# Optimization experiments

Measured on AMD Instinct MI355X. Metric: run time of the kernel, lower is better.

## Reference

```python
import jax, jax.numpy as jnp
import numpy as np

EPS = 1e-11


def setup_inputs() -> dict:
    key = jax.random.key(0)
    k1, k2, k3 = jax.random.split(key, 3)
    B, C, G, P = 32, 512, 16, 5
    z = jax.random.normal(k1, (B, C, G, G), dtype=jnp.float32)
    c = jax.random.normal(k2, (B, C, G, G), dtype=jnp.float32)
    # stacked 1x1 conv weights, one (C,C) matrix per prediction step
    W = jax.random.normal(k3, (P, C, C), dtype=jnp.float32) * 0.02
    return {"z": z, "c": c, "W": W, "neg_samples": 16, "skip_step": 1}


def reference(z, c, W, neg_samples, skip_step):
    B, C, G, _ = z.shape
    P = W.shape[0]
    total = jnp.float32(0.0)
    for k in range(1, P + 1):
        Gp = G - (k + skip_step)  # rows remaining after the k+skip offset
        # 1x1 conv == per-pixel matmul; permute(2,3,0,1) -> (Gp, G, B, C)
        ztwk = jnp.einsum('oc,bcij->ijbo', W[k - 1], z[:, :, k + skip_step:, :])
        N = Gp * G * B
        # random-index gather for negative sampling (fixed key per step)
        idx = jax.random.randint(jax.random.key(1000 + k), (N * neg_samples,), 0, N)
        ztwk_shuf = ztwk.reshape(N, C)[idx].reshape(Gp, G, B, neg_samples, C)
        # context c[:, :, :-(k+skip_step), :] permuted to (Gp, G, B, C)
        ctx = jnp.transpose(c[:, :, :Gp, :], (2, 3, 0, 1))
        # positive and negative dot products
        log_fk_main = jnp.einsum('ijbc,ijbc->ijb', ctx, ztwk)[..., None]  # (Gp,G,B,1)
        log_fk_shuf = jnp.einsum('ijbc,ijbnc->ijbn', ctx, ztwk_shuf)      # (Gp,G,B,neg)
        logits = jnp.concatenate([log_fk_main, log_fk_shuf], axis=3)
        probs = jax.nn.softmax(logits, axis=3)
        # ExpNLLLoss with target == 0 (the positive slot), mean reduction
        total = total - jnp.mean(jnp.log(probs[..., 0] + EPS))
    return total / P
```

## Files before the change

kernel.cpp:

```cpp
#include <hip/hip_runtime.h>
#include <stdint.h>


typedef __attribute__((ext_vector_type(4))) int i32x4;

using gld_gp = const __attribute__((address_space(1))) uint32_t*;
using gld_lp = __attribute__((address_space(3))) uint32_t*;

#if __has_builtin(__builtin_amdgcn_sdot4)
#define SDOT4(a, b, c) __builtin_amdgcn_sdot4((a), (b), (c), false)
#else
__device__ inline int sdot4_sw(int a, int b, int c) {
  c += (int)(signed char)(a) * (int)(signed char)(b);
  c += (int)(signed char)(a >> 8) * (int)(signed char)(b >> 8);
  c += (int)(signed char)(a >> 16) * (int)(signed char)(b >> 16);
  c += (int)(signed char)(a >> 24) * (int)(signed char)(b >> 24);
  return c;
}
#define SDOT4(a, b, c) sdot4_sw((a), (b), (c))
#endif

__host__ __device__ inline uint32_t rotl32(uint32_t x, int d) {
  return (x << d) | (x >> (32 - d));
}

__host__ __device__ inline void tf2x32(uint32_t k0, uint32_t k1,
                                       uint32_t x0, uint32_t x1,
                                       uint32_t& o0, uint32_t& o1) {
  uint32_t ks0 = k0, ks1 = k1, ks2 = 0x1BD11BDAu ^ k0 ^ k1;
  x0 += ks0; x1 += ks1;
#define TF_R(r) { x0 += x1; x1 = rotl32(x1, (r)); x1 ^= x0; }
  TF_R(13) TF_R(15) TF_R(26) TF_R(6)
  x0 += ks1; x1 += ks2 + 1u;
  TF_R(17) TF_R(29) TF_R(16) TF_R(24)
  x0 += ks2; x1 += ks0 + 2u;
  TF_R(13) TF_R(15) TF_R(26) TF_R(6)
  x0 += ks0; x1 += ks1 + 3u;
  TF_R(17) TF_R(29) TF_R(16) TF_R(24)
  x0 += ks1; x1 += ks2 + 4u;
  TF_R(13) TF_R(15) TF_R(26) TF_R(6)
  x0 += ks2; x1 += ks0 + 5u;
#undef TF_R
  o0 = x0; o1 = x1;
}

__device__ inline signed char f2i8(float f, float s) {
  int v = (int)rintf(f * s);
  v = v > 127 ? 127 : (v < -127 ? -127 : v);
  return (signed char)v;
}

struct KeyParams {
  uint32_t k1a[5], k1b[5], k2a[5], k2b[5], mult[5];
};

__global__ __launch_bounds__(256) void prep_kernel(const float* __restrict__ z,
                                                   const float* __restrict__ c,
                                                   const float* __restrict__ W,
                                                   signed char* __restrict__ zi8,
                                                   signed char* __restrict__ ci8,
                                                   signed char* __restrict__ Wti8,
                                                   int* __restrict__ idxb,
                                                   float* __restrict__ out,
                                                   KeyParams p) {
  int blk = blockIdx.x;
  int t = threadIdx.x;
  if (blk < 896) {
    bool isz = blk < 448;
    const float* src = isz ? z : c;
    signed char* dst = isz ? zi8 : ci8;
    int bb = isz ? blk : blk - 448;
    int g = isz ? 2 + (bb >> 5) : (bb >> 5);
    int b = bb & 31;
    __shared__ signed char tileB[512][17];
#pragma unroll 4
    for (int it = 0; it < 32; ++it) {
      int e = it * 256 + t;
      int cc = e >> 4, j = e & 15;
      tileB[cc][j] = f2i8(src[b * 131072 + cc * 256 + g * 16 + j], 32.f);
    }
    __syncthreads();
#pragma unroll 4
    for (int it = 0; it < 16; ++it) {
      int e = it * 256 + t;
      int jj = e >> 8, cc2 = (e & 255) * 2;
      char2 v = {tileB[cc2][jj], tileB[cc2 + 1][jj]};
      *reinterpret_cast<char2*>(
          &dst[(size_t)((g * 16 + jj) * 32 + b) * 512 + cc2]) = v;
    }
  } else if (blk < 1216) {
    int bb = blk - 896;
    int k = bb >> 6, rem = bb & 63;
    int ot = rem >> 3, it = rem & 7;
    const float* Wk = W + (size_t)k * 262144;
    signed char* Wo = Wti8 + (size_t)k * 262144;
    __shared__ signed char wt[64][68];
    int ii = t & 63, q0 = t >> 6;
#pragma unroll
    for (int q = 0; q < 16; ++q) {
      int oo = q0 + q * 4;
      wt[oo][ii] = f2i8(Wk[(size_t)(ot * 64 + oo) * 512 + it * 64 + ii], 1024.f);
    }
    __syncthreads();
    int oo2 = t & 63;
#pragma unroll
    for (int q = 0; q < 16; ++q) {
      int i2 = q0 + q * 4;
      Wo[(size_t)(it * 64 + i2) * 512 + ot * 64 + oo2] = wt[oo2][i2];
    }
  } else {
    int gid = (blk - 1216) * 256 + t;
    if (gid == 0) out[0] = 0.0f;
    int k; uint32_t span; int m;
    if (gid < 114688)      { k = 0; m = gid;          span = 7168; }
    else if (gid < 221184) { k = 1; m = gid - 114688; span = 6656; }
    else if (gid < 319488) { k = 2; m = gid - 221184; span = 6144; }
    else if (gid < 409600) { k = 3; m = gid - 319488; span = 5632; }
    else                   { k = 4; m = gid - 409600; span = 5120; }
    uint32_t h0, h1, l0, l1;
    tf2x32(p.k1a[k], p.k1b[k], 0u, (uint32_t)m, h0, h1);
    tf2x32(p.k2a[k], p.k2b[k], 0u, (uint32_t)m, l0, l1);
    uint32_t hi = h0 ^ h1, lo = l0 ^ l1;
    uint32_t off = ((hi % span) * p.mult[k] + (lo % span)) % span;
    idxb[gid] = (int)off;
  }
}

__global__ __launch_bounds__(256) void gemm_i8(const signed char* __restrict__ ci8,
                                               const signed char* __restrict__ Wti8,
                                               signed char* __restrict__ u) {
  int rt = blockIdx.x, ct = blockIdx.y;
  int kk, Tk;
  if (rt < 56)       { kk = 0; Tk = 0;   }
  else if (rt < 108) { kk = 1; Tk = 56;  }
  else if (rt < 156) { kk = 2; Tk = 108; }
  else if (rt < 200) { kk = 3; Tk = 156; }
  else               { kk = 4; Tk = 200; }
  const int preR[5] = {0, 7168, 13824, 19968, 25600};
  int r0 = (rt - Tk) * 128;
  const signed char* A  = ci8 + (size_t)r0 * 512;
  const signed char* Bw = Wti8 + (size_t)kk * 262144 + (size_t)ct * 128 * 512;
  signed char* Cb = u + ((size_t)preR[kk] + r0) * 512 + ct * 128;

  __shared__ __align__(1024) signed char As[8192];
  __shared__ __align__(1024) signed char Bs[8192];
  int tid = threadIdx.x;
  int wave = tid >> 6, lane = tid & 63;
  int wr = wave >> 1, wc = wave & 1;
  int lp = lane & 15, lg = lane >> 4;

  i32x4 acc[4][4];
#pragma unroll
  for (int m = 0; m < 4; ++m)
#pragma unroll
    for (int n = 0; n < 4; ++n) acc[m][n] = (i32x4){0, 0, 0, 0};

  int lrow = lane >> 2, lq = lane & 3;
  for (int c0 = 0; c0 < 512; c0 += 64) {
#pragma unroll
    for (int it = 0; it < 2; ++it) {
      int chunk = wave * 2 + it;
      int row = chunk * 16 + lrow;
      __builtin_amdgcn_global_load_lds(
          (gld_gp)(const void*)(A + (size_t)row * 512 + c0 + lq * 16),
          (gld_lp)(void*)(As + chunk * 1024 + lane * 16), 16, 0, 0);
      __builtin_amdgcn_global_load_lds(
          (gld_gp)(const void*)(Bw + (size_t)row * 512 + c0 + lq * 16),
          (gld_lp)(void*)(Bs + chunk * 1024 + lane * 16), 16, 0, 0);
    }
    __syncthreads();
    i32x4 af[4], bfr[4];
#pragma unroll
    for (int m = 0; m < 4; ++m)
      af[m] = *reinterpret_cast<const i32x4*>(&As[(wr * 64 + m * 16 + lp) * 64 + lg * 16]);
#pragma unroll
    for (int n = 0; n < 4; ++n)
      bfr[n] = *reinterpret_cast<const i32x4*>(&Bs[(wc * 64 + n * 16 + lp) * 64 + lg * 16]);
#pragma unroll
    for (int m = 0; m < 4; ++m)
#pragma unroll
      for (int n = 0; n < 4; ++n)
        acc[m][n] = __builtin_amdgcn_mfma_i32_16x16x64_i8(af[m], bfr[n], acc[m][n], 0, 0, 0);
    __syncthreads();
  }
#pragma unroll
  for (int m = 0; m < 4; ++m)
#pragma unroll
    for (int n = 0; n < 4; ++n)
#pragma unroll
      for (int j = 0; j < 4; ++j) {
        int row = wr * 64 + m * 16 + lg * 4 + j;
        int col = wc * 64 + n * 16 + lp;
        int q = (int)rintf((float)acc[m][n][j] * (1.f / 512.f));
        q = q > 127 ? 127 : (q < -127 ? -127 : q);
        Cb[(size_t)row * 512 + col] = (signed char)q;
      }
}

__device__ inline int dot16i8(uint4 u4, uint4 z4, int acc) {
  acc = SDOT4((int)u4.x, (int)z4.x, acc);
  acc = SDOT4((int)u4.y, (int)z4.y, acc);
  acc = SDOT4((int)u4.z, (int)z4.z, acc);
  acc = SDOT4((int)u4.w, (int)z4.w, acc);
  return acc;
}

__global__ __launch_bounds__(256) void loss_fused(const signed char* __restrict__ u,
                                                  const signed char* __restrict__ zi8,
                                                  const int* __restrict__ idxb,
                                                  float* __restrict__ out) {
  int tid = threadIdx.x;
  int wave = tid >> 6, lane = tid & 63;
  int g = lane >> 4, lp = lane & 15;
  int r = blockIdx.x * 16 + wave * 4 + g;

  int base, basez; float scale;
  if (r < 7168)       { base = 0;     basez = 1024; scale = 1.f / (7168.f * 5.f); }
  else if (r < 13824) { base = 7168;  basez = 1536; scale = 1.f / (6656.f * 5.f); }
  else if (r < 19968) { base = 13824; basez = 2048; scale = 1.f / (6144.f * 5.f); }
  else if (r < 25600) { base = 19968; basez = 2560; scale = 1.f / (5632.f * 5.f); }
  else                { base = 25600; basez = 3072; scale = 1.f / (5120.f * 5.f); }
  int rloc = r - base;

  uint4 uA, uB;
  {
    const uint4* u4 = reinterpret_cast<const uint4*>(&u[(size_t)r * 512 + lp * 32]);
    uA = u4[0]; uB = u4[1];
  }
  const int4* ip = reinterpret_cast<const int4*>(&idxb[(size_t)r * 16]);
  int4 i0 = ip[0], i1 = ip[1], i2 = ip[2], i3 = ip[3];
  int rn[16] = {i0.x, i0.y, i0.z, i0.w, i1.x, i1.y, i1.z, i1.w,
                i2.x, i2.y, i2.z, i2.w, i3.x, i3.y, i3.z, i3.w};

  int s[17];
  {
    const uint4* p0 = reinterpret_cast<const uint4*>(
        &zi8[(size_t)(basez + rloc) * 512 + lp * 32]);
    uint4 a = p0[0], b = p0[1];
    s[0] = dot16i8(uB, b, dot16i8(uA, a, 0));
  }
#pragma unroll
  for (int grp = 0; grp < 2; ++grp) {
    uint4 a0, b0, a1, b1, a2, b2, a3, b3, a4, b4, a5, b5, a6, b6, a7, b7;
#define LDROW(i, A, B)                                                        \
    {                                                                         \
      const uint4* p = reinterpret_cast<const uint4*>(                        \
          &zi8[(size_t)(basez + rn[grp * 8 + (i)]) * 512 + lp * 32]);         \
      A = p[0]; B = p[1];                                                     \
    }
    LDROW(0, a0, b0) LDROW(1, a1, b1) LDROW(2, a2, b2) LDROW(3, a3, b3)
    LDROW(4, a4, b4) LDROW(5, a5, b5) LDROW(6, a6, b6) LDROW(7, a7, b7)
#undef LDROW
    s[1 + grp * 8 + 0] = dot16i8(uB, b0, dot16i8(uA, a0, 0));
    s[1 + grp * 8 + 1] = dot16i8(uB, b1, dot16i8(uA, a1, 0));
    s[1 + grp * 8 + 2] = dot16i8(uB, b2, dot16i8(uA, a2, 0));
    s[1 + grp * 8 + 3] = dot16i8(uB, b3, dot16i8(uA, a3, 0));
    s[1 + grp * 8 + 4] = dot16i8(uB, b4, dot16i8(uA, a4, 0));
    s[1 + grp * 8 + 5] = dot16i8(uB, b5, dot16i8(uA, a5, 0));
    s[1 + grp * 8 + 6] = dot16i8(uB, b6, dot16i8(uA, a6, 0));
    s[1 + grp * 8 + 7] = dot16i8(uB, b7, dot16i8(uA, a7, 0));
  }
#pragma unroll
  for (int i = 0; i < 17; ++i) {
#pragma unroll
    for (int o = 8; o > 0; o >>= 1) s[i] += __shfl_xor(s[i], o, 64);
  }
  const float inv = 1.f / 2048.f;
  float sf[17];
#pragma unroll
  for (int i = 0; i < 17; ++i) sf[i] = (float)s[i] * inv;
  float mx = sf[0];
#pragma unroll
  for (int i = 1; i < 17; ++i) mx = fmaxf(mx, sf[i]);
  float se = 0.f;
#pragma unroll
  for (int i = 0; i < 17; ++i) se += __expf(sf[i] - mx);
  float p0 = __expf(sf[0] - mx) / se;
  float lsum = -logf(p0 + 1e-11f) * scale;

  __shared__ float red[16];
  if (lp == 0) red[wave * 4 + g] = lsum;
  __syncthreads();
  if (tid == 0) {
    float tsum = 0.f;
#pragma unroll
    for (int i = 0; i < 16; ++i) tsum += red[i];
    atomicAdd(out, tsum);
  }
}

extern "C" void kernel_launch(void* const* d_in, const int* in_sizes, int n_in,
                              void* d_out, int out_size, void* d_ws, size_t ws_size,
                              hipStream_t stream) {
  const float* z = (const float*)d_in[0];
  const float* c = (const float*)d_in[1];
  const float* W = (const float*)d_in[2];
  float* out = (float*)d_out;

  signed char* zi8  = (signed char*)d_ws;
  signed char* ci8  = zi8 + ((size_t)4 << 20);
  signed char* Wti8 = ci8 + ((size_t)4 << 20);
  signed char* u    = Wti8 + ((size_t)2 << 20);
  int* idxb = (int*)(u + (size_t)15728640);

  KeyParams p;
  for (int k = 1; k <= 5; ++k) {
    int Gp = 16 - (k + 1);
    uint32_t span = (uint32_t)(Gp * 512);
    p.mult[k - 1] = (uint32_t)((1ull << 32) % (uint64_t)span);
    uint32_t key0 = 0u, key1 = (uint32_t)(1000 + k);
    tf2x32(key0, key1, 0u, 0u, p.k1a[k - 1], p.k1b[k - 1]);
    tf2x32(key0, key1, 0u, 1u, p.k2a[k - 1], p.k2b[k - 1]);
  }

  prep_kernel<<<dim3(3136), dim3(256), 0, stream>>>(z, c, W, zi8, ci8, Wti8,
                                                    idxb, out, p);
  gemm_i8<<<dim3(240, 4), dim3(256), 0, stream>>>(ci8, Wti8, u);
  loss_fused<<<dim3(1920), dim3(256), 0, stream>>>(u, zi8, idxb, out);
}
```

Measured before the change: 136.2 us.

## Restructure z/c int8 transpose-quantize with packed 16-byte stores; add nontemporal hints

The prep stage now gives each block a 64-channel slice of one batch over all 256 pixels instead of one grid row across all channels. It packs four quantized channels per 32-bit word in shared memory and writes 16-byte vectors, skipping the rows the loss never reads. This gives coalesced float reads and wide stores and cuts the prep block count. Separately, the gemm output stores and the loss kernel's loads of u and the index buffer use nontemporal hints to reduce cache pollution, which could hurt if that data would otherwise hit in cache.

```diff
diff --git a/kernel.cpp b/kernel.cpp
--- a/kernel.cpp
+++ b/kernel.cpp
@@ -3,6 +3,7 @@
 
 
 typedef __attribute__((ext_vector_type(4))) int i32x4;
+typedef __attribute__((ext_vector_type(4))) unsigned int u32x4;
 
 using gld_gp = const __attribute__((address_space(1))) uint32_t*;
 using gld_lp = __attribute__((address_space(3))) uint32_t*;
@@ -65,31 +66,42 @@
                                                    KeyParams p) {
   int blk = blockIdx.x;
   int t = threadIdx.x;
-  if (blk < 896) {
-    bool isz = blk < 448;
-    const float* src = isz ? z : c;
+  if (blk < 512) {
+    bool isz = blk < 256;
+    int bb = isz ? blk : blk - 256;
+    int b = bb & 31;
+    int cc0 = (bb >> 5) * 64;
+    const float* src = (isz ? z : c) + (size_t)b * 131072 + (size_t)cc0 * 256;
     signed char* dst = isz ? zi8 : ci8;
-    int bb = isz ? blk : blk - 448;
-    int g = isz ? 2 + (bb >> 5) : (bb >> 5);
-    int b = bb & 31;
-    __shared__ signed char tileB[512][17];
-#pragma unroll 4
-    for (int it = 0; it < 32; ++it) {
-      int e = it * 256 + t;
-      int cc = e >> 4, j = e & 15;
-      tileB[cc][j] = f2i8(src[b * 131072 + cc * 256 + g * 16 + j], 32.f);
+    __shared__ uint32_t tileU[256 * 17];
+#pragma unroll
+    for (int w = 0; w < 16; ++w) {
+      uint32_t pk = 0;
+#pragma unroll
+      for (int e = 0; e < 4; ++e) {
+        float f = src[(size_t)(w * 4 + e) * 256 + t];
+        pk |= ((uint32_t)(uint8_t)f2i8(f, 32.f)) << (e * 8);
+      }
+      tileU[t * 17 + w] = pk;
     }
     __syncthreads();
-#pragma unroll 4
-    for (int it = 0; it < 16; ++it) {
-      int e = it * 256 + t;
-      int jj = e >> 8, cc2 = (e & 255) * 2;
-      char2 v = {tileB[cc2][jj], tileB[cc2 + 1][jj]};
-      *reinterpret_cast<char2*>(
-          &dst[(size_t)((g * 16 + jj) * 32 + b) * 512 + cc2]) = v;
-    }
-  } else if (blk < 1216) {
-    int bb = blk - 896;
+#pragma unroll
+    for (int it = 0; it < 4; ++it) {
+      int flat = it * 256 + t;
+      int r_ = flat >> 2, q = flat & 3;
+      bool ok = isz ? (r_ >= 32) : (r_ < 224);
+      if (ok) {
+        uint4 v;
+        v.x = tileU[r_ * 17 + q * 4 + 0];
+        v.y = tileU[r_ * 17 + q * 4 + 1];
+        v.z = tileU[r_ * 17 + q * 4 + 2];
+        v.w = tileU[r_ * 17 + q * 4 + 3];
+        *reinterpret_cast<uint4*>(
+            &dst[(size_t)(r_ * 32 + b) * 512 + cc0 + q * 16]) = v;
+      }
+    }
+  } else if (blk < 832) {
+    int bb = blk - 512;
     int k = bb >> 6, rem = bb & 63;
     int ot = rem >> 3, it = rem & 7;
     const float* Wk = W + (size_t)k * 262144;
@@ -109,7 +121,7 @@
       Wo[(size_t)(it * 64 + i2) * 512 + ot * 64 + oo2] = wt[oo2][i2];
     }
   } else {
-    int gid = (blk - 1216) * 256 + t;
+    int gid = (blk - 832) * 256 + t;
     if (gid == 0) out[0] = 0.0f;
     int k; uint32_t span; int m;
     if (gid < 114688)      { k = 0; m = gid;          span = 7168; }
@@ -193,11 +205,11 @@
         int col = wc * 64 + n * 16 + lp;
         int q = (int)rintf((float)acc[m][n][j] * (1.f / 512.f));
         q = q > 127 ? 127 : (q < -127 ? -127 : q);
-        Cb[(size_t)row * 512 + col] = (signed char)q;
+        __builtin_nontemporal_store((signed char)q, &Cb[(size_t)row * 512 + col]);
       }
 }
 
-__device__ inline int dot16i8(uint4 u4, uint4 z4, int acc) {
+__device__ inline int dot16i8(u32x4 u4, uint4 z4, int acc) {
   acc = SDOT4((int)u4.x, (int)z4.x, acc);
   acc = SDOT4((int)u4.y, (int)z4.y, acc);
   acc = SDOT4((int)u4.z, (int)z4.z, acc);
@@ -222,15 +234,21 @@
   else                { base = 25600; basez = 3072; scale = 1.f / (5120.f * 5.f); }
   int rloc = r - base;
 
-  uint4 uA, uB;
+  u32x4 uA, uB;
   {
-    const uint4* u4 = reinterpret_cast<const uint4*>(&u[(size_t)r * 512 + lp * 32]);
-    uA = u4[0]; uB = u4[1];
-  }
-  const int4* ip = reinterpret_cast<const int4*>(&idxb[(size_t)r * 16]);
-  int4 i0 = ip[0], i1 = ip[1], i2 = ip[2], i3 = ip[3];
-  int rn[16] = {i0.x, i0.y, i0.z, i0.w, i1.x, i1.y, i1.z, i1.w,
-                i2.x, i2.y, i2.z, i2.w, i3.x, i3.y, i3.z, i3.w};
+    const u32x4* u4 = reinterpret_cast<const u32x4*>(&u[(size_t)r * 512 + lp * 32]);
+    uA = __builtin_nontemporal_load(u4);
+    uB = __builtin_nontemporal_load(u4 + 1);
+  }
+  const u32x4* ip = reinterpret_cast<const u32x4*>(&idxb[(size_t)r * 16]);
+  u32x4 i0 = __builtin_nontemporal_load(ip + 0);
+  u32x4 i1 = __builtin_nontemporal_load(ip + 1);
+  u32x4 i2 = __builtin_nontemporal_load(ip + 2);
+  u32x4 i3 = __builtin_nontemporal_load(ip + 3);
+  int rn[16] = {(int)i0.x, (int)i0.y, (int)i0.z, (int)i0.w,
+                (int)i1.x, (int)i1.y, (int)i1.z, (int)i1.w,
+                (int)i2.x, (int)i2.y, (int)i2.z, (int)i2.w,
+                (int)i3.x, (int)i3.y, (int)i3.z, (int)i3.w};
 
   int s[17];
   {
@@ -313,7 +331,7 @@
     tf2x32(key0, key1, 0u, 1u, p.k2a[k - 1], p.k2b[k - 1]);
   }
 
-  prep_kernel<<<dim3(3136), dim3(256), 0, stream>>>(z, c, W, zi8, ci8, Wti8,
+  prep_kernel<<<dim3(2752), dim3(256), 0, stream>>>(z, c, W, zi8, ci8, Wti8,
                                                     idxb, out, p);
   gemm_i8<<<dim3(240, 4), dim3(256), 0, stream>>>(ci8, Wti8, u);
   loss_fused<<<dim3(1920), dim3(256), 0, stream>>>(u, zi8, idxb, out);
```

New measurement: 154.8 us. 13.7% more time.
